# Optimization experiments

Hardware: AMD Instinct MI355X
Metric: run time of the kernel (lower is better)

## Reference

```python
import jax, jax.numpy as jnp
import numpy as np

B, L, D = 1, 512, 1024
NH, NKV, NR = 16, 4, 16
HD, RD = 64, 64
NREP = NH // NKV  # 4
ATTN_SCALE = 1.0 / float(np.sqrt(HD))
REL_SCALE = 1.0 / float(np.sqrt(RD))


def setup_inputs() -> dict:
    key = jax.random.key(0)
    ks = jax.random.split(key, 9)
    x = jax.random.normal(ks[0], (B, L, D), jnp.float32)
    symbols = jax.random.normal(ks[1], (B, L, D), jnp.float32)
    # standard llama-style RoPE frequencies: [L, HD//2]
    inv_freq = 1.0 / (10000.0 ** (np.arange(0, HD, 2, dtype=np.float32) / HD))
    f = np.outer(np.arange(L, dtype=np.float32), inv_freq)
    freqs_cos = jnp.asarray(np.cos(f), jnp.float32)
    freqs_sin = jnp.asarray(np.sin(f), jnp.float32)
    s = 0.02
    wq_attn = jax.random.normal(ks[2], (D, NH * HD), jnp.float32) * s
    wk_attn = jax.random.normal(ks[3], (D, NKV * HD), jnp.float32) * s
    wq_rel = jax.random.normal(ks[4], (D, NR * RD), jnp.float32) * s
    wk_rel = jax.random.normal(ks[5], (D, NR * RD), jnp.float32) * s
    wr = jax.random.normal(ks[6], (NR, NH * HD), jnp.float32) * s
    wv = jax.random.normal(ks[7], (D, NKV * HD), jnp.float32) * s
    wo = jax.random.normal(ks[8], (NH * HD, NH * HD), jnp.float32) * s
    return dict(x=x, symbols=symbols, freqs_cos=freqs_cos, freqs_sin=freqs_sin,
                wq_attn=wq_attn, wk_attn=wk_attn, wq_rel=wq_rel, wk_rel=wk_rel,
                wr=wr, wv=wv, wo=wo)


def _rope(t, cos, sin):
    # t: [b, l, h, hd]; cos/sin: [l, hd//2]
    tr = t.reshape(t.shape[:-1] + (HD // 2, 2))
    re, im = tr[..., 0], tr[..., 1]
    c = cos[None, :, None, :]
    s = sin[None, :, None, :]
    out = jnp.stack([re * c - im * s, re * s + im * c], axis=-1)
    return out.reshape(t.shape)


def reference(x, symbols, freqs_cos, freqs_sin, wq_attn, wk_attn, wq_rel, wk_rel, wr, wv, wo):
    b, l, _ = x.shape
    q = (x @ wq_attn).reshape(b, l, NH, HD)
    k = (x @ wk_attn).reshape(b, l, NKV, HD)
    qr = (x @ wq_rel).reshape(b, l, NR, RD)
    kr = (x @ wk_rel).reshape(b, l, NR, RD)
    sv = (symbols @ wv).reshape(b, l, NKV, HD)
    q = _rope(q, freqs_cos, freqs_sin)
    k = _rope(k, freqs_cos, freqs_sin)
    # GQA: repeat kv heads consecutively (matches torch repeat_kv expand+reshape)
    k = jnp.repeat(k, NREP, axis=2)
    sv = jnp.repeat(sv, NREP, axis=2)
    scores = jnp.einsum('bihd,bjhd->bhij', q, k) * ATTN_SCALE
    causal = jnp.tril(jnp.ones((l, l), bool))
    scores = jnp.where(causal[None, None], scores, -jnp.inf)
    attn = jax.nn.softmax(scores, axis=-1)  # [b, nh, l, l]
    # relation scores, identity activation, laid out as [b, i, j, nr]
    relations = jnp.einsum('bird,bjrd->bijr', qr, kr) * REL_SCALE
    proj_rel = (relations @ wr).reshape(b, l, l, NH, HD)  # dominant intermediate
    attended_symbols = jnp.einsum('bhij,bjhd->bihd', attn, sv)
    attended_relations = jnp.einsum('bhij,bijhd->bihd', attn, proj_rel)
    out = (attended_symbols + attended_relations).reshape(b, l, NH * HD) @ wo
    return out, attn, relations
```

## Files before the change

kernel.cpp:

```cpp
#include <hip/hip_runtime.h>
#include <math.h>

#define ATTN_SCALE 0.125f
#define REL_SCALE 0.125f

using ushort = unsigned short;
using bf16x8 = __attribute__((ext_vector_type(8))) __bf16;
using floatx4 = __attribute__((ext_vector_type(4))) float;
using ushort8 = __attribute__((ext_vector_type(8))) ushort;
using ushort4v = __attribute__((ext_vector_type(4))) ushort;

__device__ __forceinline__ ushort f2bf(float x) {
  unsigned int u = __builtin_bit_cast(unsigned int, x);
  u += 0x7fffu + ((u >> 16) & 1u);
  return (ushort)(u >> 16);
}

__global__ __launch_bounds__(256) void prep_kernel(
    const float* __restrict__ x, const float* __restrict__ sym,
    const float* __restrict__ wq, const float* __restrict__ wk,
    const float* __restrict__ wqr, const float* __restrict__ wkr,
    const float* __restrict__ wv, const float* __restrict__ wo,
    ushort* __restrict__ xb, ushort* __restrict__ symb,
    ushort* __restrict__ wqT, ushort* __restrict__ wkT, ushort* __restrict__ wqrT,
    ushort* __restrict__ wkrT, ushort* __restrict__ wvT, ushort* __restrict__ woT) {
  if (blockIdx.z == 6) {
    int b = blockIdx.y * 32 + blockIdx.x;
    if (b >= 512) return;
    int idx = b * 256 + threadIdx.x;
    int i4 = idx << 2;
    float4 v = *(const float4*)(x + i4);
    uint2 o;
    o.x = (unsigned)f2bf(v.x) | ((unsigned)f2bf(v.y) << 16);
    o.y = (unsigned)f2bf(v.z) | ((unsigned)f2bf(v.w) << 16);
    *(uint2*)(xb + i4) = o;
    float4 w = *(const float4*)(sym + i4);
    o.x = (unsigned)f2bf(w.x) | ((unsigned)f2bf(w.y) << 16);
    o.y = (unsigned)f2bf(w.z) | ((unsigned)f2bf(w.w) << 16);
    *(uint2*)(symb + i4) = o;
    return;
  }
  __shared__ ushort t[32][33];
  const float* in;
  ushort* out;
  int N;
  switch (blockIdx.z) {
    case 0: in = wq;  out = wqT;  N = 1024; break;
    case 1: in = wk;  out = wkT;  N = 256;  break;
    case 2: in = wqr; out = wqrT; N = 1024; break;
    case 3: in = wkr; out = wkrT; N = 1024; break;
    case 4: in = wv;  out = wvT;  N = 256;  break;
    default: in = wo; out = woT;  N = 1024; break;
  }
  int n0 = blockIdx.x << 5;
  if (n0 >= N) return;
  int k0 = blockIdx.y << 5;
  int tx = threadIdx.x & 31, ty = threadIdx.x >> 5;
#pragma unroll
  for (int rr = 0; rr < 32; rr += 8)
    t[ty + rr][tx] = f2bf(in[(size_t)(k0 + ty + rr) * N + n0 + tx]);
  __syncthreads();
#pragma unroll
  for (int rr = 0; rr < 32; rr += 8)
    out[(size_t)(n0 + ty + rr) * 1024 + k0 + tx] = t[tx][ty + rr];
}

__global__ __launch_bounds__(256) void proj_mfma(
    const ushort* __restrict__ xb, const ushort* __restrict__ symb,
    const ushort* __restrict__ wqT, const ushort* __restrict__ wkT,
    const ushort* __restrict__ wqrT, const ushort* __restrict__ wkrT,
    const ushort* __restrict__ wvT,
    ushort* __restrict__ qb, ushort* __restrict__ kb, ushort* __restrict__ qrb,
    ushort* __restrict__ krb, ushort* __restrict__ svT,
    const float* __restrict__ fcos, const float* __restrict__ fsin) {
  __shared__ ushort As[64][136];
  __shared__ ushort Bs[32][136];
  const int z = blockIdx.z;
  const ushort* A = xb;
  const ushort* Bt;
  ushort* C;
  int N;
  switch (z) {
    case 0: Bt = wqT;  C = qb;  N = 1024; break;
    case 1: Bt = wkT;  C = kb;  N = 256;  break;
    case 2: Bt = wqrT; C = qrb; N = 1024; break;
    case 3: Bt = wkrT; C = krb; N = 1024; break;
    default: A = symb; Bt = wvT; C = svT; N = 256; break;
  }
  const int bn = blockIdx.x << 5;
  if (bn >= N) return;
  const int bm = blockIdx.y << 6;
  const int tid = threadIdx.x;
  const int sr = tid >> 2, sc = (tid & 3) << 5;
  const int br = tid >> 3, bc = (tid & 7) << 4;
  const int lane = tid & 63;
  const int wy = (tid >> 7) & 1, wx = (tid >> 6) & 1;
  const int lm = lane & 15, lq = lane >> 4;
  const ushort* a_rd = &As[32 * wy + lm][lq * 8];
  const ushort* b_rd = &Bs[16 * wx + lm][lq * 8];
  floatx4 acc[2] = {};
  for (int k0 = 0; k0 < 1024; k0 += 128) {
    const ushort* Ap = A + (size_t)(bm + sr) * 1024 + k0 + sc;
    ushort8 av0 = *(const ushort8*)Ap;
    ushort8 av1 = *(const ushort8*)(Ap + 8);
    ushort8 av2 = *(const ushort8*)(Ap + 16);
    ushort8 av3 = *(const ushort8*)(Ap + 24);
    const ushort* Bp = Bt + (size_t)(bn + br) * 1024 + k0 + bc;
    ushort8 bv0 = *(const ushort8*)Bp;
    ushort8 bv1 = *(const ushort8*)(Bp + 8);
    __syncthreads();
    *(ushort8*)&As[sr][sc] = av0;
    *(ushort8*)&As[sr][sc + 8] = av1;
    *(ushort8*)&As[sr][sc + 16] = av2;
    *(ushort8*)&As[sr][sc + 24] = av3;
    *(ushort8*)&Bs[br][bc] = bv0;
    *(ushort8*)&Bs[br][bc + 8] = bv1;
    __syncthreads();
#pragma unroll
    for (int kh = 0; kh < 4; ++kh) {
      bf16x8 a0 = *(const bf16x8*)(a_rd + kh * 32);
      bf16x8 a1 = *(const bf16x8*)(a_rd + 16 * 136 + kh * 32);
      bf16x8 b0 = *(const bf16x8*)(b_rd + kh * 32);
      acc[0] = __builtin_amdgcn_mfma_f32_16x16x32_bf16(a0, b0, acc[0], 0, 0, 0);
      acc[1] = __builtin_amdgcn_mfma_f32_16x16x32_bf16(a1, b0, acc[1], 0, 0, 0);
    }
  }
  if (z <= 1) {
#pragma unroll
    for (int sy = 0; sy < 2; ++sy)
#pragma unroll
      for (int e = 0; e < 4; ++e) {
        int row = bm + 32 * wy + 16 * sy + 4 * lq + e;
        int col = bn + 16 * wx + lm;
        float v = acc[sy][e];
        float pv = __shfl_xor(v, 1);
        int d = col & 63, p = d >> 1;
        float c = fcos[(row << 5) + p], s = fsin[(row << 5) + p];
        float o = (d & 1) ? fmaf(pv, s, v * c) : fmaf(v, c, -pv * s);
        C[(size_t)row * N + col] = f2bf(o);
      }
  } else if (z == 4) {
#pragma unroll
    for (int sy = 0; sy < 2; ++sy)
#pragma unroll
      for (int e = 0; e < 4; ++e) {
        int row = bm + 32 * wy + 16 * sy + 4 * lq + e;
        int col = bn + 16 * wx + lm;
        svT[(size_t)col * 512 + row] = f2bf(acc[sy][e]);
      }
  } else {
#pragma unroll
    for (int sy = 0; sy < 2; ++sy)
#pragma unroll
      for (int e = 0; e < 4; ++e) {
        int row = bm + 32 * wy + 16 * sy + 4 * lq + e;
        int col = bn + 16 * wx + lm;
        C[(size_t)row * N + col] = f2bf(acc[sy][e]);
      }
  }
}

__global__ __launch_bounds__(256) void relflash_kernel(
    const ushort* __restrict__ qb, const ushort* __restrict__ kb,
    const ushort* __restrict__ svT, const ushort* __restrict__ qrb,
    const ushort* __restrict__ krb, float* __restrict__ attn,
    ushort* __restrict__ attn_b, float* __restrict__ asym,
    float* __restrict__ rel, ushort* __restrict__ rel_bT) {
  __shared__ float S[16][516];
  __shared__ ushort P[16][520];
  const int bx = blockIdx.x;
  const int tid = threadIdx.x, wave = tid >> 6, lane = tid & 63;
  const int lm = lane & 15, lq = lane >> 4;
  if (bx >= 512) {
    const int b = bx - 512;
    const int bi0 = (b >> 4) << 5, bj0 = (b & 15) << 5;
    const int ib = bi0 + ((wave >> 1) << 4), jb = bj0 + ((wave & 1) << 4);
    const ushort* qrow = qrb + (size_t)(ib + lm) * 1024 + lq * 8;
    const ushort* krow = krb + (size_t)(jb + lm) * 1024 + lq * 8;
    floatx4 acc[16];
#pragma unroll
    for (int rq = 0; rq < 4; ++rq) {
#pragma unroll
      for (int rr = 0; rr < 4; ++rr) {
        int r = (rq << 2) + rr;
        int roff = r << 6;
        bf16x8 a0 = *(const bf16x8*)(qrow + roff);
        bf16x8 a1 = *(const bf16x8*)(qrow + roff + 32);
        bf16x8 b0 = *(const bf16x8*)(krow + roff);
        bf16x8 b1 = *(const bf16x8*)(krow + roff + 32);
        floatx4 t = {0.f, 0.f, 0.f, 0.f};
        t = __builtin_amdgcn_mfma_f32_16x16x32_bf16(a0, b0, t, 0, 0, 0);
        t = __builtin_amdgcn_mfma_f32_16x16x32_bf16(a1, b1, t, 0, 0, 0);
        acc[r] = t;
      }
    }
#pragma unroll
    for (int e = 0; e < 4; ++e) {
      int i = ib + 4 * lq + e, j = jb + lm;
      float* dst = rel + ((size_t)i * 512 + j) * 16;
      ushort* tb = rel_bT + (size_t)i * 8192 + j;
#pragma unroll
      for (int q = 0; q < 4; ++q) {
        float4 v = make_float4(acc[4 * q + 0][e] * REL_SCALE,
                               acc[4 * q + 1][e] * REL_SCALE,
                               acc[4 * q + 2][e] * REL_SCALE,
                               acc[4 * q + 3][e] * REL_SCALE);
        *(float4*)(dst + (q << 2)) = v;
        tb[(size_t)(4 * q + 0) * 512] = f2bf(v.x);
        tb[(size_t)(4 * q + 1) * 512] = f2bf(v.y);
        tb[(size_t)(4 * q + 2) * 512] = f2bf(v.z);
        tb[(size_t)(4 * q + 3) * 512] = f2bf(v.w);
      }
    }
    return;
  }
  const int h = bx >> 5, it = 31 - (bx & 31);
  const int i0 = it << 4, kv = h >> 2;
  const int ntiles = it + 1;
  const ushort* qrow = qb + (size_t)(i0 + lm) * 1024 + (h << 6) + lq * 8;
  bf16x8 a0 = *(const bf16x8*)(qrow);
  bf16x8 a1 = *(const bf16x8*)(qrow + 32);
  for (int jt = wave; jt < ntiles; jt += 4) {
    int jb = jt << 4;
    const ushort* krow = kb + (size_t)(jb + lm) * 256 + (kv << 6) + lq * 8;
    bf16x8 b0 = *(const bf16x8*)(krow);
    bf16x8 b1 = *(const bf16x8*)(krow + 32);
    floatx4 acc = {0.f, 0.f, 0.f, 0.f};
    acc = __builtin_amdgcn_mfma_f32_16x16x32_bf16(a0, b0, acc, 0, 0, 0);
    acc = __builtin_amdgcn_mfma_f32_16x16x32_bf16(a1, b1, acc, 0, 0, 0);
#pragma unroll
    for (int e = 0; e < 4; ++e) S[4 * lq + e][jb + lm] = acc[e] * ATTN_SCALE;
  }
  __syncthreads();
  const int row = tid >> 4, t16 = tid & 15;
  const int i = i0 + row;
  const int nj = ntiles << 4;
  float m = -INFINITY;
  for (int s = 0; (s << 6) < nj; ++s) {
    int j4 = (t16 << 2) + (s << 6);
    float4 v = *(const float4*)&S[row][j4];
    if (j4 + 0 <= i) m = fmaxf(m, v.x);
    if (j4 + 1 <= i) m = fmaxf(m, v.y);
    if (j4 + 2 <= i) m = fmaxf(m, v.z);
    if (j4 + 3 <= i) m = fmaxf(m, v.w);
  }
#pragma unroll
  for (int o = 8; o; o >>= 1) m = fmaxf(m, __shfl_xor(m, o, 16));
  float sum = 0.f;
  for (int s = 0; (s << 6) < nj; ++s) {
    int j4 = (t16 << 2) + (s << 6);
    float4 v = *(const float4*)&S[row][j4];
    v.x = (j4 + 0 <= i) ? __expf(v.x - m) : 0.f;
    v.y = (j4 + 1 <= i) ? __expf(v.y - m) : 0.f;
    v.z = (j4 + 2 <= i) ? __expf(v.z - m) : 0.f;
    v.w = (j4 + 3 <= i) ? __expf(v.w - m) : 0.f;
    sum += v.x + v.y + v.z + v.w;
    *(float4*)&S[row][j4] = v;
  }
#pragma unroll
  for (int o = 8; o; o >>= 1) sum += __shfl_xor(sum, o, 16);
  const float inv = 1.f / sum;
  float* arow = attn + (size_t)h * 262144 + (size_t)i * 512;
  ushort* abrow = attn_b + (size_t)i * 8192 + (size_t)h * 512;
  for (int s = 0; s < 8; ++s) {
    int j4 = (t16 << 2) + (s << 6);
    float4 o4 = {0.f, 0.f, 0.f, 0.f};
    if (j4 < nj) {
      float4 v = *(const float4*)&S[row][j4];
      o4.x = v.x * inv;
      o4.y = v.y * inv;
      o4.z = v.z * inv;
      o4.w = v.w * inv;
    }
    *(float4*)(arow + j4) = o4;
    ushort4v p4;
    p4.x = f2bf(o4.x); p4.y = f2bf(o4.y); p4.z = f2bf(o4.z); p4.w = f2bf(o4.w);
    *(ushort4v*)&P[row][j4] = p4;
    *(ushort4v*)(abrow + j4) = p4;
  }
  __syncthreads();
  const int dbase = wave << 4;
  floatx4 acc2 = {0.f, 0.f, 0.f, 0.f};
  const ushort* svrow = svT + (size_t)((kv << 6) + dbase + lm) * 512;
  const int kmax = (nj + 31) & ~31;
  for (int kt = 0; kt < kmax; kt += 32) {
    bf16x8 pa = *(const bf16x8*)&P[lm][kt + lq * 8];
    bf16x8 pb = *(const bf16x8*)(svrow + kt + lq * 8);
    acc2 = __builtin_amdgcn_mfma_f32_16x16x32_bf16(pa, pb, acc2, 0, 0, 0);
  }
#pragma unroll
  for (int e = 0; e < 4; ++e)
    asym[(size_t)(i0 + 4 * lq + e) * 1024 + (h << 6) + dbase + lm] = acc2[e];
}

__global__ __launch_bounds__(256) void tker_combine(const ushort* __restrict__ attn_b,
                                                    const ushort* __restrict__ rel_bT,
                                                    const float* __restrict__ asym,
                                                    const float* __restrict__ wr,
                                                    ushort* __restrict__ attb) {
  const int i = blockIdx.x;
  const int tid = threadIdx.x, wave = tid >> 6, lane = tid & 63;
  const int lm = lane & 15, lq = lane >> 4;
  __shared__ float Ts[4][16][17];
  floatx4 acc = {0.f, 0.f, 0.f, 0.f};
  const ushort* arow = attn_b + (size_t)i * 8192 + (size_t)lm * 512;
  const ushort* brow = rel_bT + (size_t)i * 8192 + (size_t)lm * 512;
  const int ktiles = (i >> 5) + 1;
  for (int kt = wave; kt < ktiles; kt += 4) {
    int k = (kt << 5) + lq * 8;
    bf16x8 a = *(const bf16x8*)(arow + k);
    bf16x8 b = *(const bf16x8*)(brow + k);
    acc = __builtin_amdgcn_mfma_f32_16x16x32_bf16(a, b, acc, 0, 0, 0);
  }
#pragma unroll
  for (int e = 0; e < 4; ++e) Ts[wave][4 * lq + e][lm] = acc[e];
  __syncthreads();
  const int hc = tid >> 4, d4 = (tid & 15) << 2;
  float4 o = *(const float4*)(asym + (size_t)i * 1024 + (hc << 6) + d4);
#pragma unroll
  for (int rr = 0; rr < 16; ++rr) {
    float tv = Ts[0][hc][rr] + Ts[1][hc][rr] + Ts[2][hc][rr] + Ts[3][hc][rr];
    float4 w4 = *(const float4*)(wr + (size_t)rr * 1024 + (hc << 6) + d4);
    o.x = fmaf(tv, w4.x, o.x);
    o.y = fmaf(tv, w4.y, o.y);
    o.z = fmaf(tv, w4.z, o.z);
    o.w = fmaf(tv, w4.w, o.w);
  }
  ushort4v ob;
  ob.x = f2bf(o.x); ob.y = f2bf(o.y); ob.z = f2bf(o.z); ob.w = f2bf(o.w);
  *(ushort4v*)(attb + (size_t)i * 1024 + (hc << 6) + d4) = ob;
}

__global__ __launch_bounds__(256) void out_mfma(const ushort* __restrict__ attb,
                                                const ushort* __restrict__ woT,
                                                float* __restrict__ out) {
  __shared__ ushort As[64][136];
  __shared__ ushort Bs[32][136];
  const int bn = blockIdx.x << 5, bm = blockIdx.y << 6;
  const int tid = threadIdx.x;
  const int sr = tid >> 2, sc = (tid & 3) << 5;
  const int br = tid >> 3, bc = (tid & 7) << 4;
  const int lane = tid & 63;
  const int wy = (tid >> 7) & 1, wx = (tid >> 6) & 1;
  const int lm = lane & 15, lq = lane >> 4;
  const ushort* a_rd = &As[32 * wy + lm][lq * 8];
  const ushort* b_rd = &Bs[16 * wx + lm][lq * 8];
  floatx4 acc[2] = {};
  for (int k0 = 0; k0 < 1024; k0 += 128) {
    const ushort* Ap = attb + (size_t)(bm + sr) * 1024 + k0 + sc;
    ushort8 av0 = *(const ushort8*)Ap;
    ushort8 av1 = *(const ushort8*)(Ap + 8);
    ushort8 av2 = *(const ushort8*)(Ap + 16);
    ushort8 av3 = *(const ushort8*)(Ap + 24);
    const ushort* Bp = woT + (size_t)(bn + br) * 1024 + k0 + bc;
    ushort8 bv0 = *(const ushort8*)Bp;
    ushort8 bv1 = *(const ushort8*)(Bp + 8);
    __syncthreads();
    *(ushort8*)&As[sr][sc] = av0;
    *(ushort8*)&As[sr][sc + 8] = av1;
    *(ushort8*)&As[sr][sc + 16] = av2;
    *(ushort8*)&As[sr][sc + 24] = av3;
    *(ushort8*)&Bs[br][bc] = bv0;
    *(ushort8*)&Bs[br][bc + 8] = bv1;
    __syncthreads();
#pragma unroll
    for (int kh = 0; kh < 4; ++kh) {
      bf16x8 a0 = *(const bf16x8*)(a_rd + kh * 32);
      bf16x8 a1 = *(const bf16x8*)(a_rd + 16 * 136 + kh * 32);
      bf16x8 b0 = *(const bf16x8*)(b_rd + kh * 32);
      acc[0] = __builtin_amdgcn_mfma_f32_16x16x32_bf16(a0, b0, acc[0], 0, 0, 0);
      acc[1] = __builtin_amdgcn_mfma_f32_16x16x32_bf16(a1, b0, acc[1], 0, 0, 0);
    }
  }
#pragma unroll
  for (int sy = 0; sy < 2; ++sy)
#pragma unroll
    for (int e = 0; e < 4; ++e) {
      int row = bm + 32 * wy + 16 * sy + 4 * lq + e;
      int col = bn + 16 * wx + lm;
      out[(size_t)row * 1024 + col] = acc[sy][e];
    }
}

extern "C" void kernel_launch(void* const* d_in, const int* in_sizes, int n_in,
                              void* d_out, int out_size, void* d_ws, size_t ws_size,
                              hipStream_t stream) {
  const float* x       = (const float*)d_in[0];
  const float* symbols = (const float*)d_in[1];
  const float* fcos    = (const float*)d_in[2];
  const float* fsin    = (const float*)d_in[3];
  const float* wq_attn = (const float*)d_in[4];
  const float* wk_attn = (const float*)d_in[5];
  const float* wq_rel  = (const float*)d_in[6];
  const float* wk_rel  = (const float*)d_in[7];
  const float* wr      = (const float*)d_in[8];
  const float* wv      = (const float*)d_in[9];
  const float* wo      = (const float*)d_in[10];

  float* out  = (float*)d_out;
  float* attn = out + 524288;
  float* rel  = attn + 4194304;

  char* wsb = (char*)d_ws;
  const size_t KB = 1024;
  ushort* xb     = (ushort*)(wsb);
  ushort* symb   = (ushort*)(wsb + 1024 * KB);
  ushort* wqT    = (ushort*)(wsb + 2048 * KB);
  ushort* wkT    = (ushort*)(wsb + 4096 * KB);
  ushort* wqrT   = (ushort*)(wsb + 4608 * KB);
  ushort* wkrT   = (ushort*)(wsb + 6656 * KB);
  ushort* wvT    = (ushort*)(wsb + 8704 * KB);
  ushort* woT    = (ushort*)(wsb + 9216 * KB);
  ushort* qb     = (ushort*)(wsb + 11264 * KB);
  ushort* kb     = (ushort*)(wsb + 12288 * KB);
  ushort* qrb    = (ushort*)(wsb + 12544 * KB);
  ushort* krb    = (ushort*)(wsb + 13568 * KB);
  ushort* svT    = (ushort*)(wsb + 14592 * KB);
  float*  asym   = (float*)(wsb + 14848 * KB);
  ushort* attb   = (ushort*)(wsb + 16896 * KB);
  ushort* rel_bT = (ushort*)(wsb + 17920 * KB);
  ushort* attn_b = (ushort*)(wsb + 26112 * KB);

  prep_kernel<<<dim3(32, 32, 7), 256, 0, stream>>>(x, symbols, wq_attn, wk_attn,
                                                   wq_rel, wk_rel, wv, wo,
                                                   xb, symb, wqT, wkT, wqrT, wkrT, wvT, woT);
  proj_mfma<<<dim3(32, 8, 5), 256, 0, stream>>>(xb, symb, wqT, wkT, wqrT, wkrT, wvT,
                                                qb, kb, qrb, krb, svT, fcos, fsin);
  relflash_kernel<<<dim3(768), 256, 0, stream>>>(qb, kb, svT, qrb, krb, attn, attn_b,
                                                 asym, rel, rel_bT);
  tker_combine<<<dim3(512), 256, 0, stream>>>(attn_b, rel_bT, asym, wr, attb);
  out_mfma<<<dim3(32, 8), 256, 0, stream>>>(attb, woT, out);
}
```

Before: 148.4 us.

## Vectorize weight transpose, stage rel_bT via LDS, double-accumulate combine loop

```diff
diff --git a/kernel.cpp b/kernel.cpp
--- a/kernel.cpp
+++ b/kernel.cpp
@@ -40,7 +40,7 @@
     *(uint2*)(symb + i4) = o;
     return;
   }
-  __shared__ ushort t[32][33];
+  __shared__ ushort t[32][44];
   const float* in;
   ushort* out;
   int N;
@@ -55,14 +55,23 @@
   int n0 = blockIdx.x << 5;
   if (n0 >= N) return;
   int k0 = blockIdx.y << 5;
-  int tx = threadIdx.x & 31, ty = threadIdx.x >> 5;
-#pragma unroll
-  for (int rr = 0; rr < 32; rr += 8)
-    t[ty + rr][tx] = f2bf(in[(size_t)(k0 + ty + rr) * N + n0 + tx]);
+  {
+    int kr = threadIdx.x >> 3, nq = threadIdx.x & 7;
+    float4 v = *(const float4*)(in + (size_t)(k0 + kr) * N + n0 + (nq << 2));
+    ushort4v c;
+    c.x = f2bf(v.x); c.y = f2bf(v.y); c.z = f2bf(v.z); c.w = f2bf(v.w);
+    *(ushort4v*)&t[kr][nq << 2] = c;
+  }
   __syncthreads();
-#pragma unroll
-  for (int rr = 0; rr < 32; rr += 8)
-    out[(size_t)(n0 + ty + rr) * 1024 + k0 + tx] = t[tx][ty + rr];
+  {
+    int nr = threadIdx.x >> 3, kq = threadIdx.x & 7;
+    ushort4v c;
+    c.x = t[(kq << 2) + 0][nr];
+    c.y = t[(kq << 2) + 1][nr];
+    c.z = t[(kq << 2) + 2][nr];
+    c.w = t[(kq << 2) + 3][nr];
+    *(ushort4v*)(out + (size_t)(n0 + nr) * 1024 + k0 + (kq << 2)) = c;
+  }
 }
 
 __global__ __launch_bounds__(256) void proj_mfma(
@@ -160,14 +169,22 @@
   }
 }
 
+struct FlashSh {
+  float S[16][516];
+  ushort P[16][520];
+};
+union RelFlashSh {
+  FlashSh f;
+  ushort RT[32 * 648];
+};
+
 __global__ __launch_bounds__(256) void relflash_kernel(
     const ushort* __restrict__ qb, const ushort* __restrict__ kb,
     const ushort* __restrict__ svT, const ushort* __restrict__ qrb,
     const ushort* __restrict__ krb, float* __restrict__ attn,
     ushort* __restrict__ attn_b, float* __restrict__ asym,
     float* __restrict__ rel, ushort* __restrict__ rel_bT) {
-  __shared__ float S[16][516];
-  __shared__ ushort P[16][520];
+  __shared__ RelFlashSh sh;
   const int bx = blockIdx.x;
   const int tid = threadIdx.x, wave = tid >> 6, lane = tid & 63;
   const int lm = lane & 15, lq = lane >> 4;
@@ -175,6 +192,7 @@
     const int b = bx - 512;
     const int bi0 = (b >> 4) << 5, bj0 = (b & 15) << 5;
     const int ib = bi0 + ((wave >> 1) << 4), jb = bj0 + ((wave & 1) << 4);
+    const int il0 = (wave >> 1) << 4, jl0 = (wave & 1) << 4;
     const ushort* qrow = qrb + (size_t)(ib + lm) * 1024 + lq * 8;
     const ushort* krow = krb + (size_t)(jb + lm) * 1024 + lq * 8;
     floatx4 acc[16];
@@ -197,8 +215,9 @@
 #pragma unroll
     for (int e = 0; e < 4; ++e) {
       int i = ib + 4 * lq + e, j = jb + lm;
+      int il = il0 + 4 * lq + e, jl = jl0 + lm;
       float* dst = rel + ((size_t)i * 512 + j) * 16;
-      ushort* tb = rel_bT + (size_t)i * 8192 + j;
+      ushort* rt = &sh.RT[il * 648 + jl];
 #pragma unroll
       for (int q = 0; q < 4; ++q) {
         float4 v = make_float4(acc[4 * q + 0][e] * REL_SCALE,
@@ -206,10 +225,21 @@
                                acc[4 * q + 2][e] * REL_SCALE,
                                acc[4 * q + 3][e] * REL_SCALE);
         *(float4*)(dst + (q << 2)) = v;
-        tb[(size_t)(4 * q + 0) * 512] = f2bf(v.x);
-        tb[(size_t)(4 * q + 1) * 512] = f2bf(v.y);
-        tb[(size_t)(4 * q + 2) * 512] = f2bf(v.z);
-        tb[(size_t)(4 * q + 3) * 512] = f2bf(v.w);
+        rt[(4 * q + 0) * 40] = f2bf(v.x);
+        rt[(4 * q + 1) * 40] = f2bf(v.y);
+        rt[(4 * q + 2) * 40] = f2bf(v.z);
+        rt[(4 * q + 3) * 40] = f2bf(v.w);
+      }
+    }
+    __syncthreads();
+    {
+      const int r = lane >> 2, jq = lane & 3;
+#pragma unroll
+      for (int it2 = 0; it2 < 8; ++it2) {
+        int il = (it2 << 2) + wave;
+        ushort8 v = *(const ushort8*)&sh.RT[il * 648 + r * 40 + (jq << 3)];
+        *(ushort8*)(rel_bT + (size_t)(bi0 + il) * 8192 + (size_t)r * 512 + bj0 +
+                    (jq << 3)) = v;
       }
     }
     return;
@@ -229,7 +259,7 @@
     acc = __builtin_amdgcn_mfma_f32_16x16x32_bf16(a0, b0, acc, 0, 0, 0);
     acc = __builtin_amdgcn_mfma_f32_16x16x32_bf16(a1, b1, acc, 0, 0, 0);
 #pragma unroll
-    for (int e = 0; e < 4; ++e) S[4 * lq + e][jb + lm] = acc[e] * ATTN_SCALE;
+    for (int e = 0; e < 4; ++e) sh.f.S[4 * lq + e][jb + lm] = acc[e] * ATTN_SCALE;
   }
   __syncthreads();
   const int row = tid >> 4, t16 = tid & 15;
@@ -238,7 +268,7 @@
   float m = -INFINITY;
   for (int s = 0; (s << 6) < nj; ++s) {
     int j4 = (t16 << 2) + (s << 6);
-    float4 v = *(const float4*)&S[row][j4];
+    float4 v = *(const float4*)&sh.f.S[row][j4];
     if (j4 + 0 <= i) m = fmaxf(m, v.x);
     if (j4 + 1 <= i) m = fmaxf(m, v.y);
     if (j4 + 2 <= i) m = fmaxf(m, v.z);
@@ -249,13 +279,13 @@
   float sum = 0.f;
   for (int s = 0; (s << 6) < nj; ++s) {
     int j4 = (t16 << 2) + (s << 6);
-    float4 v = *(const float4*)&S[row][j4];
+    float4 v = *(const float4*)&sh.f.S[row][j4];
     v.x = (j4 + 0 <= i) ? __expf(v.x - m) : 0.f;
     v.y = (j4 + 1 <= i) ? __expf(v.y - m) : 0.f;
     v.z = (j4 + 2 <= i) ? __expf(v.z - m) : 0.f;
     v.w = (j4 + 3 <= i) ? __expf(v.w - m) : 0.f;
     sum += v.x + v.y + v.z + v.w;
-    *(float4*)&S[row][j4] = v;
+    *(float4*)&sh.f.S[row][j4] = v;
   }
 #pragma unroll
   for (int o = 8; o; o >>= 1) sum += __shfl_xor(sum, o, 16);
@@ -266,7 +296,7 @@
     int j4 = (t16 << 2) + (s << 6);
     float4 o4 = {0.f, 0.f, 0.f, 0.f};
     if (j4 < nj) {
-      float4 v = *(const float4*)&S[row][j4];
+      float4 v = *(const float4*)&sh.f.S[row][j4];
       o4.x = v.x * inv;
       o4.y = v.y * inv;
       o4.z = v.z * inv;
@@ -275,7 +305,7 @@
     *(float4*)(arow + j4) = o4;
     ushort4v p4;
     p4.x = f2bf(o4.x); p4.y = f2bf(o4.y); p4.z = f2bf(o4.z); p4.w = f2bf(o4.w);
-    *(ushort4v*)&P[row][j4] = p4;
+    *(ushort4v*)&sh.f.P[row][j4] = p4;
     *(ushort4v*)(abrow + j4) = p4;
   }
   __syncthreads();
@@ -284,7 +314,7 @@
   const ushort* svrow = svT + (size_t)((kv << 6) + dbase + lm) * 512;
   const int kmax = (nj + 31) & ~31;
   for (int kt = 0; kt < kmax; kt += 32) {
-    bf16x8 pa = *(const bf16x8*)&P[lm][kt + lq * 8];
+    bf16x8 pa = *(const bf16x8*)&sh.f.P[lm][kt + lq * 8];
     bf16x8 pb = *(const bf16x8*)(svrow + kt + lq * 8);
     acc2 = __builtin_amdgcn_mfma_f32_16x16x32_bf16(pa, pb, acc2, 0, 0, 0);
   }
@@ -302,18 +332,29 @@
   const int tid = threadIdx.x, wave = tid >> 6, lane = tid & 63;
   const int lm = lane & 15, lq = lane >> 4;
   __shared__ float Ts[4][16][17];
-  floatx4 acc = {0.f, 0.f, 0.f, 0.f};
+  floatx4 acc0 = {0.f, 0.f, 0.f, 0.f}, acc1 = {0.f, 0.f, 0.f, 0.f};
   const ushort* arow = attn_b + (size_t)i * 8192 + (size_t)lm * 512;
   const ushort* brow = rel_bT + (size_t)i * 8192 + (size_t)lm * 512;
   const int ktiles = (i >> 5) + 1;
-  for (int kt = wave; kt < ktiles; kt += 4) {
-    int k = (kt << 5) + lq * 8;
-    bf16x8 a = *(const bf16x8*)(arow + k);
-    bf16x8 b = *(const bf16x8*)(brow + k);
-    acc = __builtin_amdgcn_mfma_f32_16x16x32_bf16(a, b, acc, 0, 0, 0);
-  }
-#pragma unroll
-  for (int e = 0; e < 4; ++e) Ts[wave][4 * lq + e][lm] = acc[e];
+  int kt = wave;
+  for (; kt + 4 < ktiles; kt += 8) {
+    int k0 = (kt << 5) + lq * 8, k1 = ((kt + 4) << 5) + lq * 8;
+    bf16x8 a0 = *(const bf16x8*)(arow + k0);
+    bf16x8 b0 = *(const bf16x8*)(brow + k0);
+    bf16x8 a1 = *(const bf16x8*)(arow + k1);
+    bf16x8 b1 = *(const bf16x8*)(brow + k1);
+    acc0 = __builtin_amdgcn_mfma_f32_16x16x32_bf16(a0, b0, acc0, 0, 0, 0);
+    acc1 = __builtin_amdgcn_mfma_f32_16x16x32_bf16(a1, b1, acc1, 0, 0, 0);
+  }
+  if (kt < ktiles) {
+    int k0 = (kt << 5) + lq * 8;
+    bf16x8 a0 = *(const bf16x8*)(arow + k0);
+    bf16x8 b0 = *(const bf16x8*)(brow + k0);
+    acc0 = __builtin_amdgcn_mfma_f32_16x16x32_bf16(a0, b0, acc0, 0, 0, 0);
+  }
+  acc0 = acc0 + acc1;
+#pragma unroll
+  for (int e = 0; e < 4; ++e) Ts[wave][4 * lq + e][lm] = acc0[e];
   __syncthreads();
   const int hc = tid >> 4, d4 = (tid & 15) << 2;
   float4 o = *(const float4*)(asym + (size_t)i * 1024 + (hc << 6) + d4);
```

Measured after the change: 146.1 us. About the same (-1.6%).
